# Kernel tuning notes

Measured on AMD Instinct MI355X. Metric: run time of the kernel, lower is better.

Reference implementation:

```python
import jax, jax.numpy as jnp
import numpy as np

N = 16384
E = 262144
S = 8
F = 32  # ECCConv channels


def _ecc(x, src, tgt, e, Wk, bk, root, b):
    # Edge-conditioned conv (Spektral ECCConv, single mode):
    # per-edge filter from edge features, gather-matmul-scatter, root transform.
    n = x.shape[0]
    fin = x.shape[1]
    filt = (e @ Wk + bk).reshape(e.shape[0], fin, F)      # (E, F_in, F_out)
    msg = jnp.einsum('ei,eio->eo', x[src], filt)           # (E, F_out)
    agg = jax.ops.segment_sum(msg, tgt, num_segments=n)    # (N, F_out)
    return jax.nn.relu(agg + x @ root + b)


def setup_inputs() -> dict:
    key = jax.random.key(0)
    ks = jax.random.split(key, 10)
    x = jax.random.normal(ks[0], (N, 33), dtype=jnp.float32)
    x = x.at[:, -1].set(1.0)  # mask column
    src = jax.random.randint(ks[1], (E,), 0, N, dtype=jnp.int32)
    tgt = jax.random.randint(ks[2], (E,), 0, N, dtype=jnp.int32)
    e = jax.random.normal(ks[3], (E, S), dtype=jnp.float32)
    def w(k, shape, fan_in):
        return jax.random.normal(k, shape, dtype=jnp.float32) * (1.0 / np.sqrt(fan_in))
    return {
        'x': x, 'src': src, 'tgt': tgt, 'e': e,
        'Wk1': w(ks[4], (S, F * F), S), 'bk1': jnp.zeros((F * F,), jnp.float32),
        'root1': w(ks[5], (F, F), F), 'b1': jnp.zeros((F,), jnp.float32),
        'Wk2': w(ks[6], (S, F * F), S), 'bk2': jnp.zeros((F * F,), jnp.float32),
        'root2': w(ks[7], (F, F), F), 'b2': jnp.zeros((F,), jnp.float32),
        'Wd': w(ks[8], (F, 1), F), 'bd': jnp.zeros((1,), jnp.float32),
    }


def reference(x, src, tgt, e, Wk1, bk1, root1, b1, Wk2, bk2, root2, b2, Wd, bd):
    h = x[:, :-1]  # GraphMasking: strip mask column -> (N, 32)
    h = _ecc(h, src, tgt, e, Wk1, bk1, root1, b1)
    h = _ecc(h, src, tgt, e, Wk2, bk2, root2, b2)
    pooled = jnp.sum(h, axis=0, keepdims=True)  # GlobalSumPool -> (1, 32)
    out = jax.nn.relu(pooled @ Wd + bd)          # Dense(1, relu) -> (1, 1)
    return out
```

## Files before the change

### kernel.cpp

```cpp
#include <hip/hip_runtime.h>

#define NN 16384
#define NE 262144

__global__ __launch_bounds__(256) void prep_kernel(
    const float* __restrict__ hin, int in_stride, int apply_relu,
    const float* __restrict__ Wk, const float* __restrict__ bk,
    const float* __restrict__ root, const float* __restrict__ bvec,
    float* __restrict__ G, float* __restrict__ agg, int n)
{
    int gtid = blockIdx.x * blockDim.x + threadIdx.x;
    int wid  = gtid >> 6;
    int nw   = (gridDim.x * blockDim.x) >> 6;
    int lane = threadIdx.x & 63;
    int o    = lane & 31;
    int half = lane >> 5;

    float w[5][32];
#pragma unroll
    for (int k = 0; k < 5; ++k) {
        int s = half * 5 + k;
        const float* Ws = (s < 8) ? (Wk + s * 1024) : ((s == 8) ? bk : root);
#pragma unroll
        for (int i = 0; i < 32; ++i) w[k][i] = Ws[i * 32 + o];
    }
    float bo = bvec[o];

    for (int v = wid; v < n; v += nw) {
        float hv = hin[(size_t)v * in_stride + o];
        if (apply_relu) hv = fmaxf(hv, 0.0f);
        float acc0 = 0.f, acc1 = 0.f, acc2 = 0.f, acc3 = 0.f, acc4 = 0.f;
#pragma unroll
        for (int i = 0; i < 32; ++i) {
            float hi = __shfl(hv, i, 64);
            acc0 = fmaf(hi, w[0][i], acc0);
            acc1 = fmaf(hi, w[1][i], acc1);
            acc2 = fmaf(hi, w[2][i], acc2);
            acc3 = fmaf(hi, w[3][i], acc3);
            acc4 = fmaf(hi, w[4][i], acc4);
        }
        float* Gv = G + (size_t)v * 288;
        if (half == 0) {
            Gv[0 * 32 + o] = acc0;
            Gv[1 * 32 + o] = acc1;
            Gv[2 * 32 + o] = acc2;
            Gv[3 * 32 + o] = acc3;
            Gv[4 * 32 + o] = acc4;
        } else {
            Gv[5 * 32 + o] = acc0;
            Gv[6 * 32 + o] = acc1;
            Gv[7 * 32 + o] = acc2;
            Gv[8 * 32 + o] = acc3;
            agg[(size_t)v * 32 + o] = acc4 + bo;
        }
    }
}

__global__ __launch_bounds__(256) void edge_kernel(
    const float* __restrict__ efeat, const int* __restrict__ src,
    const int* __restrict__ tgt, const float* __restrict__ G,
    float* __restrict__ agg, int ne)
{
    int gtid = blockIdx.x * blockDim.x + threadIdx.x;
    int o    = gtid & 31;
    int hw   = gtid >> 5;
    int nhw  = (gridDim.x * blockDim.x) >> 5;

    for (int ei = hw; ei < ne; ei += nhw) {
        int s = src[ei];
        int t = tgt[ei];
        const float4* pe = (const float4*)(efeat + (size_t)ei * 8);
        float4 ea = pe[0];
        float4 eb = pe[1];
        const float* g = G + (size_t)s * 288;
        float m = g[8 * 32 + o];
        m = fmaf(ea.x, g[0 * 32 + o], m);
        m = fmaf(ea.y, g[1 * 32 + o], m);
        m = fmaf(ea.z, g[2 * 32 + o], m);
        m = fmaf(ea.w, g[3 * 32 + o], m);
        m = fmaf(eb.x, g[4 * 32 + o], m);
        m = fmaf(eb.y, g[5 * 32 + o], m);
        m = fmaf(eb.z, g[6 * 32 + o], m);
        m = fmaf(eb.w, g[7 * 32 + o], m);
        atomicAdd(agg + (size_t)t * 32 + o, m);
    }
}

__global__ void init_pooled(float* __restrict__ pooled)
{
    int t = threadIdx.x;
    if (t < 32) pooled[t] = 0.0f;
}

__global__ __launch_bounds__(256) void pool_kernel(
    const float* __restrict__ agg, float* __restrict__ pooled, int n)
{
    int gtid  = blockIdx.x * blockDim.x + threadIdx.x;
    int o     = gtid & 31;
    int row0  = gtid >> 5;
    int nrows = (gridDim.x * blockDim.x) >> 5;
    float sum = 0.0f;
    for (int v = row0; v < n; v += nrows)
        sum += fmaxf(agg[(size_t)v * 32 + o], 0.0f);
    sum += __shfl_xor(sum, 32, 64);
    if ((threadIdx.x & 63) < 32) atomicAdd(pooled + o, sum);
}

__global__ void final_kernel(const float* __restrict__ pooled,
                             const float* __restrict__ Wd,
                             const float* __restrict__ bd,
                             float* __restrict__ out)
{
    int lane = threadIdx.x;
    float v = (lane < 32) ? pooled[lane] * Wd[lane] : 0.0f;
#pragma unroll
    for (int k = 32; k >= 1; k >>= 1) v += __shfl_xor(v, k, 64);
    if (lane == 0) out[0] = fmaxf(v + bd[0], 0.0f);
}

extern "C" void kernel_launch(void* const* d_in, const int* in_sizes, int n_in,
                              void* d_out, int out_size, void* d_ws, size_t ws_size,
                              hipStream_t stream)
{
    const float* x     = (const float*)d_in[0];
    const int*   src   = (const int*)d_in[1];
    const int*   tgt   = (const int*)d_in[2];
    const float* e     = (const float*)d_in[3];
    const float* Wk1   = (const float*)d_in[4];
    const float* bk1   = (const float*)d_in[5];
    const float* root1 = (const float*)d_in[6];
    const float* b1    = (const float*)d_in[7];
    const float* Wk2   = (const float*)d_in[8];
    const float* bk2   = (const float*)d_in[9];
    const float* root2 = (const float*)d_in[10];
    const float* b2    = (const float*)d_in[11];
    const float* Wd    = (const float*)d_in[12];
    const float* bd    = (const float*)d_in[13];
    float* out = (float*)d_out;

    char*  ws     = (char*)d_ws;
    float* agg    = (float*)ws;
    float* pooled = (float*)(ws + (size_t)NN * 32 * 4);
    float* G      = (float*)(ws + (size_t)NN * 32 * 4 + 256);

    init_pooled<<<1, 64, 0, stream>>>(pooled);

    prep_kernel<<<512, 256, 0, stream>>>(x, 33, 0, Wk1, bk1, root1, b1, G, agg, NN);
    edge_kernel<<<8192, 256, 0, stream>>>(e, src, tgt, G, agg, NE);

    prep_kernel<<<512, 256, 0, stream>>>(agg, 32, 1, Wk2, bk2, root2, b2, G, agg, NN);
    edge_kernel<<<8192, 256, 0, stream>>>(e, src, tgt, G, agg, NE);

    pool_kernel<<<64, 256, 0, stream>>>(agg, pooled, NN);
    final_kernel<<<1, 64, 0, stream>>>(pooled, Wd, bd, out);
}
```

Baseline: 143.9 us.

## Sort edges by source into CSR and aggregate per source node

Builds a source-sorted CSR on every call (histogram, a single-block scan, an atomic scatter of targets and edge features). The edge kernels are replaced by a per-source-node kernel that loads the node's 9x32 G slice once into registers and loops over its edges. This removes the repeated random 1152-byte G gathers per edge. In exchange it adds four preprocessing launches, a serial single-block scan, and an extra read and write of the edge features. Atomic scatter to targets remains, and per-node loop lengths are imbalanced.

```diff
diff --git a/kernel.cpp b/kernel.cpp
--- a/kernel.cpp
+++ b/kernel.cpp
@@ -56,40 +56,105 @@
     }
 }
 
-__global__ __launch_bounds__(256) void edge_kernel(
-    const float* __restrict__ efeat, const int* __restrict__ src,
-    const int* __restrict__ tgt, const float* __restrict__ G,
-    float* __restrict__ agg, int ne)
+__global__ __launch_bounds__(256) void zero_misc(int* __restrict__ cnt,
+                                                 float* __restrict__ pooled)
+{
+    int i = blockIdx.x * blockDim.x + threadIdx.x;
+    if (i < NN) cnt[i] = 0;
+    if (i < 32) pooled[i] = 0.0f;
+}
+
+__global__ __launch_bounds__(256) void hist_kernel(const int* __restrict__ src,
+                                                   int* __restrict__ cnt)
+{
+    int i = blockIdx.x * blockDim.x + threadIdx.x;
+    if (i < NE) atomicAdd(&cnt[src[i]], 1);
+}
+
+__global__ __launch_bounds__(1024) void scan_kernel(int* __restrict__ cnt,
+                                                    int* __restrict__ offs)
+{
+    __shared__ int a[1024], b[1024];
+    int t = threadIdx.x;
+    int base = t * 16;
+    int local[16];
+    int s = 0;
+#pragma unroll
+    for (int j = 0; j < 16; ++j) { local[j] = s; s += cnt[base + j]; }
+    a[t] = s;
+    __syncthreads();
+    int* in  = a;
+    int* out = b;
+    for (int off = 1; off < 1024; off <<= 1) {
+        out[t] = in[t] + ((t >= off) ? in[t - off] : 0);
+        __syncthreads();
+        int* tmp = in; in = out; out = tmp;
+    }
+    int excl = (t == 0) ? 0 : in[t - 1];
+#pragma unroll
+    for (int j = 0; j < 16; ++j) { offs[base + j] = excl + local[j]; cnt[base + j] = 0; }
+    if (t == 1023) offs[NN] = in[1023];
+}
+
+__global__ __launch_bounds__(256) void scatter_kernel(
+    const int* __restrict__ src, const int* __restrict__ tgt,
+    const float* __restrict__ e, const int* __restrict__ offs,
+    int* __restrict__ cnt, int* __restrict__ tgt_s, float* __restrict__ e_s)
+{
+    int i = blockIdx.x * blockDim.x + threadIdx.x;
+    if (i < NE) {
+        int sv = src[i];
+        int pos = offs[sv] + atomicAdd(&cnt[sv], 1);
+        tgt_s[pos] = tgt[i];
+        const float4* pe = (const float4*)(e + (size_t)i * 8);
+        float4 ea = pe[0];
+        float4 eb = pe[1];
+        float4* po = (float4*)(e_s + (size_t)pos * 8);
+        po[0] = ea;
+        po[1] = eb;
+    }
+}
+
+__global__ __launch_bounds__(256) void agg_src_kernel(
+    const float* __restrict__ e_s, const int* __restrict__ tgt_s,
+    const int* __restrict__ offs, const float* __restrict__ G,
+    float* __restrict__ agg, int n)
 {
     int gtid = blockIdx.x * blockDim.x + threadIdx.x;
     int o    = gtid & 31;
     int hw   = gtid >> 5;
     int nhw  = (gridDim.x * blockDim.x) >> 5;
 
-    for (int ei = hw; ei < ne; ei += nhw) {
-        int s = src[ei];
-        int t = tgt[ei];
-        const float4* pe = (const float4*)(efeat + (size_t)ei * 8);
-        float4 ea = pe[0];
-        float4 eb = pe[1];
-        const float* g = G + (size_t)s * 288;
-        float m = g[8 * 32 + o];
-        m = fmaf(ea.x, g[0 * 32 + o], m);
-        m = fmaf(ea.y, g[1 * 32 + o], m);
-        m = fmaf(ea.z, g[2 * 32 + o], m);
-        m = fmaf(ea.w, g[3 * 32 + o], m);
-        m = fmaf(eb.x, g[4 * 32 + o], m);
-        m = fmaf(eb.y, g[5 * 32 + o], m);
-        m = fmaf(eb.z, g[6 * 32 + o], m);
-        m = fmaf(eb.w, g[7 * 32 + o], m);
-        atomicAdd(agg + (size_t)t * 32 + o, m);
-    }
-}
-
-__global__ void init_pooled(float* __restrict__ pooled)
-{
-    int t = threadIdx.x;
-    if (t < 32) pooled[t] = 0.0f;
+    for (int v = hw; v < n; v += nhw) {
+        const float* g = G + (size_t)v * 288;
+        float g0 = g[0 * 32 + o];
+        float g1 = g[1 * 32 + o];
+        float g2 = g[2 * 32 + o];
+        float g3 = g[3 * 32 + o];
+        float g4 = g[4 * 32 + o];
+        float g5 = g[5 * 32 + o];
+        float g6 = g[6 * 32 + o];
+        float g7 = g[7 * 32 + o];
+        float g8 = g[8 * 32 + o];
+        int beg = offs[v];
+        int end = offs[v + 1];
+        for (int ed = beg; ed < end; ++ed) {
+            const float4* pe = (const float4*)(e_s + (size_t)ed * 8);
+            float4 ea = pe[0];
+            float4 eb = pe[1];
+            int t = tgt_s[ed];
+            float m = g8;
+            m = fmaf(ea.x, g0, m);
+            m = fmaf(ea.y, g1, m);
+            m = fmaf(ea.z, g2, m);
+            m = fmaf(ea.w, g3, m);
+            m = fmaf(eb.x, g4, m);
+            m = fmaf(eb.y, g5, m);
+            m = fmaf(eb.z, g6, m);
+            m = fmaf(eb.w, g7, m);
+            atomicAdd(agg + (size_t)t * 32 + o, m);
+        }
+    }
 }
 
 __global__ __launch_bounds__(256) void pool_kernel(
@@ -138,18 +203,26 @@
     const float* bd    = (const float*)d_in[13];
     float* out = (float*)d_out;
 
-    char*  ws     = (char*)d_ws;
-    float* agg    = (float*)ws;
-    float* pooled = (float*)(ws + (size_t)NN * 32 * 4);
-    float* G      = (float*)(ws + (size_t)NN * 32 * 4 + 256);
-
-    init_pooled<<<1, 64, 0, stream>>>(pooled);
+    char* ws = (char*)d_ws;
+    size_t off = 0;
+    float* agg    = (float*)(ws + off); off += (size_t)NN * 32 * 4;
+    float* pooled = (float*)(ws + off); off += 256;
+    float* G      = (float*)(ws + off); off += (size_t)NN * 288 * 4;
+    int*   cnt    = (int*)  (ws + off); off += (size_t)NN * 4;
+    int*   offs   = (int*)  (ws + off); off += ((size_t)NN + 64) * 4;
+    int*   tgt_s  = (int*)  (ws + off); off += (size_t)NE * 4;
+    float* e_s    = (float*)(ws + off); off += (size_t)NE * 8 * 4;
+
+    zero_misc<<<64, 256, 0, stream>>>(cnt, pooled);
+    hist_kernel<<<1024, 256, 0, stream>>>(src, cnt);
+    scan_kernel<<<1, 1024, 0, stream>>>(cnt, offs);
+    scatter_kernel<<<1024, 256, 0, stream>>>(src, tgt, e, offs, cnt, tgt_s, e_s);
 
     prep_kernel<<<512, 256, 0, stream>>>(x, 33, 0, Wk1, bk1, root1, b1, G, agg, NN);
-    edge_kernel<<<8192, 256, 0, stream>>>(e, src, tgt, G, agg, NE);
+    agg_src_kernel<<<2048, 256, 0, stream>>>(e_s, tgt_s, offs, G, agg, NN);
 
     prep_kernel<<<512, 256, 0, stream>>>(agg, 32, 1, Wk2, bk2, root2, b2, G, agg, NN);
-    edge_kernel<<<8192, 256, 0, stream>>>(e, src, tgt, G, agg, NE);
+    agg_src_kernel<<<2048, 256, 0, stream>>>(e_s, tgt_s, offs, G, agg, NN);
 
     pool_kernel<<<64, 256, 0, stream>>>(agg, pooled, NN);
     final_kernel<<<1, 64, 0, stream>>>(pooled, Wd, bd, out);
```

After: 167.9 us. +16.7%, slower.

## Partition node and edge work by source bucket per XCD; fuse pool and final

Applied to the files above, without the earlier changes.

Nodes are split into 8 buckets selected by blockIdx&7, so both the prep and edge kernels handle one bucket of G rows per block group. Each edge wave scans its edge groups and uses a ballot to process only edges whose source falls in its bucket, two edges per wave. On round-robin XCD dispatch this is meant to keep each bucket's roughly 2.4 MB of G rows resident in one XCD's L2, cutting the cost of the random per-edge gathers. In exchange every bucket re-reads the full src/tgt arrays, and there is divergence from the ballot loop. The pooled-sum init moves into prep_kernel, and pooling and the final dense layer are fused into one kernel using a last-block ticket, removing two small launches.

```diff
diff --git a/kernel.cpp b/kernel.cpp
--- a/kernel.cpp
+++ b/kernel.cpp
@@ -2,19 +2,29 @@
 
 #define NN 16384
 #define NE 262144
+#define NBUCKET 8
+#define BUCKET_SHIFT 11
+#define BUCKET_SZ 2048
 
 __global__ __launch_bounds__(256) void prep_kernel(
     const float* __restrict__ hin, int in_stride, int apply_relu,
     const float* __restrict__ Wk, const float* __restrict__ bk,
     const float* __restrict__ root, const float* __restrict__ bvec,
-    float* __restrict__ G, float* __restrict__ agg, int n)
+    float* __restrict__ G, float* __restrict__ agg,
+    float* __restrict__ pooled, int* __restrict__ ticket)
 {
-    int gtid = blockIdx.x * blockDim.x + threadIdx.x;
-    int wid  = gtid >> 6;
-    int nw   = (gridDim.x * blockDim.x) >> 6;
+    if (blockIdx.x == 0 && threadIdx.x < 33) {
+        if (threadIdx.x < 32) pooled[threadIdx.x] = 0.0f;
+        else *ticket = 0;
+    }
+
     int lane = threadIdx.x & 63;
     int o    = lane & 31;
     int half = lane >> 5;
+
+    int bucket = blockIdx.x & 7;
+    int wave_in_b  = (blockIdx.x >> 3) * (blockDim.x >> 6) + (threadIdx.x >> 6);
+    int waves_per_b = (gridDim.x >> 3) * (blockDim.x >> 6);
 
     float w[5][32];
 #pragma unroll
@@ -26,7 +36,8 @@
     }
     float bo = bvec[o];
 
-    for (int v = wid; v < n; v += nw) {
+    int vend = (bucket + 1) * BUCKET_SZ;
+    for (int v = bucket * BUCKET_SZ + wave_in_b; v < vend; v += waves_per_b) {
         float hv = hin[(size_t)v * in_stride + o];
         if (apply_relu) hv = fmaxf(hv, 0.0f);
         float acc0 = 0.f, acc1 = 0.f, acc2 = 0.f, acc3 = 0.f, acc4 = 0.f;
@@ -59,63 +70,83 @@
 __global__ __launch_bounds__(256) void edge_kernel(
     const float* __restrict__ efeat, const int* __restrict__ src,
     const int* __restrict__ tgt, const float* __restrict__ G,
-    float* __restrict__ agg, int ne)
+    float* __restrict__ agg)
 {
-    int gtid = blockIdx.x * blockDim.x + threadIdx.x;
-    int o    = gtid & 31;
-    int hw   = gtid >> 5;
-    int nhw  = (gridDim.x * blockDim.x) >> 5;
+    int lane = threadIdx.x & 63;
+    int o    = lane & 31;
+    int half = lane >> 5;
 
-    for (int ei = hw; ei < ne; ei += nhw) {
-        int s = src[ei];
-        int t = tgt[ei];
-        const float4* pe = (const float4*)(efeat + (size_t)ei * 8);
-        float4 ea = pe[0];
-        float4 eb = pe[1];
-        const float* g = G + (size_t)s * 288;
-        float m = g[8 * 32 + o];
-        m = fmaf(ea.x, g[0 * 32 + o], m);
-        m = fmaf(ea.y, g[1 * 32 + o], m);
-        m = fmaf(ea.z, g[2 * 32 + o], m);
-        m = fmaf(ea.w, g[3 * 32 + o], m);
-        m = fmaf(eb.x, g[4 * 32 + o], m);
-        m = fmaf(eb.y, g[5 * 32 + o], m);
-        m = fmaf(eb.z, g[6 * 32 + o], m);
-        m = fmaf(eb.w, g[7 * 32 + o], m);
-        atomicAdd(agg + (size_t)t * 32 + o, m);
+    int bucket = blockIdx.x & 7;
+    int wave_in_b  = (blockIdx.x >> 3) * (blockDim.x >> 6) + (threadIdx.x >> 6);
+    int waves_per_b = (gridDim.x >> 3) * (blockDim.x >> 6);
+
+    const int ngroups = NE / 64;
+    for (int grp = wave_in_b; grp < ngroups; grp += waves_per_b) {
+        int ebase = grp * 64;
+        int my_src = src[ebase + lane];
+        int my_tgt = tgt[ebase + lane];
+        unsigned long long ball = __ballot((my_src >> BUCKET_SHIFT) == bucket);
+        while (ball) {
+            int j0 = __ffsll(ball) - 1;
+            ball &= ball - 1;
+            int j1 = -1;
+            if (ball) { j1 = __ffsll(ball) - 1; ball &= ball - 1; }
+            int ej = half ? j1 : j0;
+            bool active = (ej >= 0);
+            int sj = active ? ej : 0;
+            int s_v = __shfl(my_src, sj, 64);
+            int t_v = __shfl(my_tgt, sj, 64);
+            if (active) {
+                const float4* pe = (const float4*)(efeat + (size_t)(ebase + ej) * 8);
+                float4 ea = pe[0];
+                float4 eb = pe[1];
+                const float* g = G + (size_t)s_v * 288;
+                float m = g[8 * 32 + o];
+                m = fmaf(ea.x, g[0 * 32 + o], m);
+                m = fmaf(ea.y, g[1 * 32 + o], m);
+                m = fmaf(ea.z, g[2 * 32 + o], m);
+                m = fmaf(ea.w, g[3 * 32 + o], m);
+                m = fmaf(eb.x, g[4 * 32 + o], m);
+                m = fmaf(eb.y, g[5 * 32 + o], m);
+                m = fmaf(eb.z, g[6 * 32 + o], m);
+                m = fmaf(eb.w, g[7 * 32 + o], m);
+                atomicAdd(agg + (size_t)t_v * 32 + o, m);
+            }
+        }
     }
 }
 
-__global__ void init_pooled(float* __restrict__ pooled)
-{
-    int t = threadIdx.x;
-    if (t < 32) pooled[t] = 0.0f;
-}
-
-__global__ __launch_bounds__(256) void pool_kernel(
-    const float* __restrict__ agg, float* __restrict__ pooled, int n)
+__global__ __launch_bounds__(256) void poolfinal_kernel(
+    const float* __restrict__ agg, const float* __restrict__ Wd,
+    const float* __restrict__ bd, float* __restrict__ pooled,
+    int* __restrict__ ticket, float* __restrict__ out)
 {
     int gtid  = blockIdx.x * blockDim.x + threadIdx.x;
     int o     = gtid & 31;
     int row0  = gtid >> 5;
     int nrows = (gridDim.x * blockDim.x) >> 5;
     float sum = 0.0f;
-    for (int v = row0; v < n; v += nrows)
+    for (int v = row0; v < NN; v += nrows)
         sum += fmaxf(agg[(size_t)v * 32 + o], 0.0f);
     sum += __shfl_xor(sum, 32, 64);
     if ((threadIdx.x & 63) < 32) atomicAdd(pooled + o, sum);
-}
+    __threadfence();
+    __syncthreads();
 
-__global__ void final_kernel(const float* __restrict__ pooled,
-                             const float* __restrict__ Wd,
-                             const float* __restrict__ bd,
-                             float* __restrict__ out)
-{
-    int lane = threadIdx.x;
-    float v = (lane < 32) ? pooled[lane] * Wd[lane] : 0.0f;
+    __shared__ int last;
+    if (threadIdx.x == 0) {
+        int old = atomicAdd(ticket, 1);
+        last = (old == (int)gridDim.x - 1) ? 1 : 0;
+    }
+    __syncthreads();
+    if (last && threadIdx.x < 64) {
+        float pv = 0.0f;
+        if (threadIdx.x < 32)
+            pv = atomicAdd(pooled + threadIdx.x, 0.0f) * Wd[threadIdx.x];
 #pragma unroll
-    for (int k = 32; k >= 1; k >>= 1) v += __shfl_xor(v, k, 64);
-    if (lane == 0) out[0] = fmaxf(v + bd[0], 0.0f);
+        for (int k = 32; k >= 1; k >>= 1) pv += __shfl_xor(pv, k, 64);
+        if (threadIdx.x == 0) out[0] = fmaxf(pv + bd[0], 0.0f);
+    }
 }
 
 extern "C" void kernel_launch(void* const* d_in, const int* in_sizes, int n_in,
@@ -138,19 +169,17 @@
     const float* bd    = (const float*)d_in[13];
     float* out = (float*)d_out;
 
-    char*  ws     = (char*)d_ws;
+    char* ws = (char*)d_ws;
     float* agg    = (float*)ws;
     float* pooled = (float*)(ws + (size_t)NN * 32 * 4);
+    int*   ticket = (int*)  (ws + (size_t)NN * 32 * 4 + 32 * 4);
     float* G      = (float*)(ws + (size_t)NN * 32 * 4 + 256);
 
-    init_pooled<<<1, 64, 0, stream>>>(pooled);
+    prep_kernel<<<512, 256, 0, stream>>>(x, 33, 0, Wk1, bk1, root1, b1, G, agg, pooled, ticket);
+    edge_kernel<<<2048, 256, 0, stream>>>(e, src, tgt, G, agg);
 
-    prep_kernel<<<512, 256, 0, stream>>>(x, 33, 0, Wk1, bk1, root1, b1, G, agg, NN);
-    edge_kernel<<<8192, 256, 0, stream>>>(e, src, tgt, G, agg, NE);
+    prep_kernel<<<512, 256, 0, stream>>>(agg, 32, 1, Wk2, bk2, root2, b2, G, agg, pooled, ticket);
+    edge_kernel<<<2048, 256, 0, stream>>>(e, src, tgt, G, agg);
 
-    prep_kernel<<<512, 256, 0, stream>>>(agg, 32, 1, Wk2, bk2, root2, b2, G, agg, NN);
-    edge_kernel<<<8192, 256, 0, stream>>>(e, src, tgt, G, agg, NE);
-
-    pool_kernel<<<64, 256, 0, stream>>>(agg, pooled, NN);
-    final_kernel<<<1, 64, 0, stream>>>(pooled, Wd, bd, out);
+    poolfinal_kernel<<<64, 256, 0, stream>>>(agg, Wd, bd, pooled, ticket, out);
 }
```

Result: faster. 120.2 us (-16.5%).
